# Kernel optimization log

Measured on AMD Instinct MI355X. Metric: run time of the kernel, lower is better.

The kernel has to match this reference:

```python
import math
import jax, jax.numpy as jnp
import numpy as np

B, D, N, KP1 = 64, 128, 500000, 4096  # batch, input_size, output_size, K+1
MOMENTUM = 0.5


def setup_inputs() -> dict:
    key = jax.random.key(0)
    k0, k1, k2, k3, k4, k5 = jax.random.split(key, 6)
    stdv = 1.0 / math.sqrt(D / 3)
    image = jax.random.normal(k0, (B, D), jnp.float32)
    gene = jax.random.normal(k1, (B, D), jnp.float32)
    index = jax.random.randint(k2, (B,), 0, N, dtype=jnp.int32)
    idx = jax.random.randint(k3, (B, KP1), 0, N, dtype=jnp.int32)
    idx = idx.at[:, 0].set(index)  # positive sample in slot 0
    memory_image = jax.random.uniform(k4, (N, D), jnp.float32) * (2 * stdv) - stdv
    memory_gene = jax.random.uniform(k5, (N, D), jnp.float32) * (2 * stdv) - stdv
    return {"image": image, "gene": gene, "memory_image": memory_image,
            "memory_gene": memory_gene, "index": index, "idx": idx}


def _momentum_update(mem, x, index):
    # gather positive rows, momentum blend, L2 normalize, scatter back
    pos = mem[index] * MOMENTUM + x * (1.0 - MOMENTUM)          # [B, D]
    pos = pos / jnp.sqrt(jnp.sum(pos * pos, axis=1, keepdims=True))
    return mem.at[index].set(pos)


def reference(image, gene, memory_image, memory_gene, index, idx):
    # gathered bank rows are detached in the original (weights .detach())
    w_gene = jax.lax.stop_gradient(memory_gene[idx])    # [B, K+1, D]
    w_image = jax.lax.stop_gradient(memory_image[idx])  # [B, K+1, D]
    # bmm([B,K+1,D], [B,D,1]) -> scores [B, K+1]; use_softmax=False branch:
    # stabilized softmax over the K+1 candidates (no temperature division)
    out_image = jax.nn.softmax(jnp.einsum('bkd,bd->bk', w_gene, image), axis=1)
    out_gene = jax.nn.softmax(jnp.einsum('bkd,bd->bk', w_image, gene), axis=1)
    # no_grad momentum scatter-update of the banks
    new_mem_image = _momentum_update(memory_image, jax.lax.stop_gradient(image), index)
    new_mem_gene = _momentum_update(memory_gene, jax.lax.stop_gradient(gene), index)
    return out_image, out_gene, new_mem_image, new_mem_gene
```

## Files before the change

### kernel.cpp

```cpp
#include <hip/hip_runtime.h>
#include <math.h>

constexpr int Bb   = 64;
constexpr int Dd   = 128;
constexpr int KP1  = 4096;
constexpr long NMEM = 500000L * 128;
constexpr int BK   = Bb * KP1;

constexpr long HALF_F4    = NMEM / 4;
constexpr int  CHUNK_F4   = 8192;
constexpr int  FULL_PER_B = 1953;
constexpr long TAIL_BASE  = (long)FULL_PER_B * CHUNK_F4;
constexpr int  TAIL_F4    = (int)(HALF_F4 - TAIL_BASE);
constexpr int  CHUNKS_PER_BANK = FULL_PER_B + 1;
constexpr int  NCHUNK     = 2 * CHUNKS_PER_BANK;

typedef float f4 __attribute__((ext_vector_type(4)));


__device__ __forceinline__ float dot8(float4 a, float4 b, float4 x0, float4 x1) {
    return a.x*x0.x + a.y*x0.y + a.z*x0.z + a.w*x0.w
         + b.x*x1.x + b.y*x1.y + b.z*x1.z + b.w*x1.w;
}

__global__ __launch_bounds__(64) void zero_ctr(unsigned* ctr) {
    if (threadIdx.x == 0) *ctr = 0u;
}

__global__ __launch_bounds__(512, 2) void fused_scores_copy(
    const float* __restrict__ image, const float* __restrict__ gene,
    const float* __restrict__ mem_image, const float* __restrict__ mem_gene,
    const int* __restrict__ idx, float* __restrict__ out, unsigned* __restrict__ ctr)
{
    const int tid = threadIdx.x;

    if (blockIdx.x < 128) {
        const int b     = blockIdx.x >> 1;
        const int which = blockIdx.x & 1;
        const float* w = which ? mem_image : mem_gene;
        const float* x = which ? gene : image;
        float* o = out + (long)which * BK + (long)b * KP1;

        __shared__ int   sidx[KP1];
        __shared__ float sv[KP1];
        __shared__ float red[8];

        {
            const int4* s4 = (const int4*)(idx + (long)b * KP1);
            int4* d4 = (int4*)sidx;
            d4[tid]       = s4[tid];
            d4[tid + 512] = s4[tid + 512];
        }

        const int lg  = tid & 15;
        const int grp = tid >> 4;

        float4 x0 = *(const float4*)(x + b * Dd + lg * 8);
        float4 x1 = *(const float4*)(x + b * Dd + lg * 8 + 4);
        __syncthreads();

        for (int j = 0; j < 128; j += 4) {
            const int k0 = grp + (j + 0) * 32;
            const int k1 = grp + (j + 1) * 32;
            const int k2 = grp + (j + 2) * 32;
            const int k3 = grp + (j + 3) * 32;
            const float4* r0 = (const float4*)(w + (long)sidx[k0] * Dd + lg * 8);
            const float4* r1 = (const float4*)(w + (long)sidx[k1] * Dd + lg * 8);
            const float4* r2 = (const float4*)(w + (long)sidx[k2] * Dd + lg * 8);
            const float4* r3 = (const float4*)(w + (long)sidx[k3] * Dd + lg * 8);
            float4 a0 = r0[0], b0 = r0[1];
            float4 a1 = r1[0], b1 = r1[1];
            float4 a2 = r2[0], b2 = r2[1];
            float4 a3 = r3[0], b3 = r3[1];
            float d0 = dot8(a0, b0, x0, x1);
            float d1 = dot8(a1, b1, x0, x1);
            float d2 = dot8(a2, b2, x0, x1);
            float d3 = dot8(a3, b3, x0, x1);
            d0 += __shfl_xor(d0, 1); d1 += __shfl_xor(d1, 1);
            d2 += __shfl_xor(d2, 1); d3 += __shfl_xor(d3, 1);
            d0 += __shfl_xor(d0, 2); d1 += __shfl_xor(d1, 2);
            d2 += __shfl_xor(d2, 2); d3 += __shfl_xor(d3, 2);
            d0 += __shfl_xor(d0, 4); d1 += __shfl_xor(d1, 4);
            d2 += __shfl_xor(d2, 4); d3 += __shfl_xor(d3, 4);
            d0 += __shfl_xor(d0, 8); d1 += __shfl_xor(d1, 8);
            d2 += __shfl_xor(d2, 8); d3 += __shfl_xor(d3, 8);
            if (lg == 0) {
                sv[k0] = d0; sv[k1] = d1; sv[k2] = d2; sv[k3] = d3;
            }
        }
        __syncthreads();

        float m = fmaxf(sv[tid], sv[tid + 512]);
        m = fmaxf(m, fmaxf(sv[tid + 1024], sv[tid + 1536]));
        m = fmaxf(m, fmaxf(sv[tid + 2048], sv[tid + 2560]));
        m = fmaxf(m, fmaxf(sv[tid + 3072], sv[tid + 3584]));
        #pragma unroll
        for (int off = 1; off < 64; off <<= 1) m = fmaxf(m, __shfl_xor(m, off));
        if ((tid & 63) == 0) red[tid >> 6] = m;
        __syncthreads();
        if (tid < 64) {
            float tv = (tid < 8) ? red[tid] : -INFINITY;
            #pragma unroll
            for (int off = 1; off < 8; off <<= 1) tv = fmaxf(tv, __shfl_xor(tv, off));
            if (tid == 0) red[0] = tv;
        }
        __syncthreads();
        m = red[0];
        __syncthreads();

        float sum = 0.f;
        #pragma unroll
        for (int r = 0; r < 8; ++r) {
            int k = tid + r * 512;
            float e = expf(sv[k] - m);
            sv[k] = e;
            sum += e;
        }
        #pragma unroll
        for (int off = 1; off < 64; off <<= 1) sum += __shfl_xor(sum, off);
        if ((tid & 63) == 0) red[tid >> 6] = sum;
        __syncthreads();
        if (tid < 64) {
            float tv = (tid < 8) ? red[tid] : 0.f;
            #pragma unroll
            for (int off = 1; off < 8; off <<= 1) tv += __shfl_xor(tv, off);
            if (tid == 0) red[0] = tv;
        }
        __syncthreads();
        const float inv = 1.0f / red[0];
        #pragma unroll
        for (int r = 0; r < 8; ++r) {
            int k = tid + r * 512;
            o[k] = sv[k] * inv;
        }
    }

    const f4* srcI = (const f4*)mem_image;
    const f4* srcG = (const f4*)mem_gene;
    f4* dst = (f4*)(out + 2 * BK);

    __shared__ unsigned sc;
    for (;;) {
        if (tid == 0) sc = atomicAdd(ctr, 1u);
        __syncthreads();
        const unsigned c = sc;
        __syncthreads();
        if (c >= NCHUNK) break;

        const int  bank  = (c < CHUNKS_PER_BANK) ? 0 : 1;
        const int  local = bank ? (int)(c - CHUNKS_PER_BANK) : (int)c;
        const f4*  sbank = bank ? srcG : srcI;
        const long dbank = (long)bank * HALF_F4;

        if (local < FULL_PER_B) {
            const long base = (long)local * CHUNK_F4;
            f4 v[16];
            #pragma unroll
            for (int k = 0; k < 16; ++k) v[k] = sbank[base + k * 512 + tid];
            #pragma unroll
            for (int k = 0; k < 16; ++k)
                __builtin_nontemporal_store(v[k], dst + dbank + base + k * 512 + tid);
        } else {
            f4 v0 = sbank[TAIL_BASE + tid];
            f4 v1 = sbank[TAIL_BASE + 512 + tid];
            __builtin_nontemporal_store(v0, dst + dbank + TAIL_BASE + tid);
            __builtin_nontemporal_store(v1, dst + dbank + TAIL_BASE + 512 + tid);
        }
    }
}

__global__ __launch_bounds__(128) void momentum_update(
    const float* __restrict__ image, const float* __restrict__ gene,
    const float* __restrict__ mem_image, const float* __restrict__ mem_gene,
    const int* __restrict__ index, float* __restrict__ out)
{
    const int b     = blockIdx.x;
    const int which = blockIdx.y;
    const float* mem = which ? mem_gene : mem_image;
    const float* x   = which ? gene : image;
    float* o = out + 2 * BK + (long)which * NMEM;

    const long row = index[b];
    const int d = threadIdx.x;

    float p = mem[row * Dd + d] * 0.5f + x[(long)b * Dd + d] * 0.5f;
    float ss = p * p;
    #pragma unroll
    for (int off = 1; off < 64; off <<= 1) ss += __shfl_xor(ss, off);
    __shared__ float r2[2];
    if ((d & 63) == 0) r2[d >> 6] = ss;
    __syncthreads();
    const float inv = 1.0f / sqrtf(r2[0] + r2[1]);
    o[row * Dd + d] = p * inv;
}

extern "C" void kernel_launch(void* const* d_in, const int* in_sizes, int n_in,
                              void* d_out, int out_size, void* d_ws, size_t ws_size,
                              hipStream_t stream) {
    const float* image     = (const float*)d_in[0];
    const float* gene      = (const float*)d_in[1];
    const float* mem_image = (const float*)d_in[2];
    const float* mem_gene  = (const float*)d_in[3];
    const int*   index     = (const int*)d_in[4];
    const int*   idx       = (const int*)d_in[5];
    float* out = (float*)d_out;
    unsigned* ctr = (unsigned*)d_ws;

    zero_ctr<<<dim3(1), 64, 0, stream>>>(ctr);
    fused_scores_copy<<<dim3(2048), 512, 0, stream>>>(
        image, gene, mem_image, mem_gene, idx, out, ctr);
    momentum_update<<<dim3(64, 2), 128, 0, stream>>>(
        image, gene, mem_image, mem_gene, index, out);
}
```

Baseline: 215.6 us.

## Fuse score dots into bank streaming copy via inverted index of idx

Adds a path that builds an inverted index from each memory row to the (batch, slot) entries that reference it, capped at 16 entries per row. Dot products are then computed while each row is already in registers during the full bank copy, and a separate softmax kernel follows. This is meant to remove the separate random gather of the sampled rows. In exchange it adds atomics, extra launches and a large workspace, and it silently drops references to any row sampled more than 16 times. The old path is kept as a fallback when the workspace is too small.

```diff
diff --git a/kernel.cpp b/kernel.cpp
--- a/kernel.cpp
+++ b/kernel.cpp
@@ -4,24 +4,160 @@
 constexpr int Bb   = 64;
 constexpr int Dd   = 128;
 constexpr int KP1  = 4096;
-constexpr long NMEM = 500000L * 128;
+constexpr int Nrow = 500000;
+constexpr long NMEM = (long)Nrow * Dd;
 constexpr int BK   = Bb * KP1;
+
+constexpr int MSLOT = 16;
+constexpr int NGROUP = 31250;
+constexpr int GPB    = 15625;
+constexpr long WS_NEED = (long)Nrow * 4 * (1 + MSLOT);
+
+typedef float f4 __attribute__((ext_vector_type(4)));
+
+__device__ __forceinline__ float dot8(float4 a, float4 b, float4 x0, float4 x1) {
+    return a.x*x0.x + a.y*x0.y + a.z*x0.z + a.w*x0.w
+         + b.x*x1.x + b.y*x1.y + b.z*x1.z + b.w*x1.w;
+}
+
+
+__global__ __launch_bounds__(512) void zero_cnt(int* cnt) {
+    int i = blockIdx.x * 512 + threadIdx.x;
+    for (; i < Nrow; i += gridDim.x * 512) cnt[i] = 0;
+}
+
+__global__ __launch_bounds__(512) void build_inv(
+    const int* __restrict__ idx, int* __restrict__ cnt, int* __restrict__ entries)
+{
+    const int j = blockIdx.x * 512 + threadIdx.x;
+    const int r = idx[j];
+    const int c = atomicAdd(&cnt[r], 1);
+    if (c < MSLOT) entries[r * MSLOT + c] = j;
+}
+
+__global__ __launch_bounds__(512, 2) void copy_score(
+    const float* __restrict__ image, const float* __restrict__ gene,
+    const float* __restrict__ mem_image, const float* __restrict__ mem_gene,
+    const int* __restrict__ cnt, const int* __restrict__ entries,
+    float* __restrict__ out)
+{
+    const int tid  = threadIdx.x;
+    const int half = tid >> 5;
+    const int lane = tid & 31;
+
+    __shared__ f4 lxi[2048];
+    __shared__ f4 lxg[2048];
+    {
+        const f4* gi = (const f4*)image;
+        const f4* gg = (const f4*)gene;
+        #pragma unroll
+        for (int u = 0; u < 4; ++u) {
+            lxi[u * 512 + tid] = gi[u * 512 + tid];
+            lxg[u * 512 + tid] = gg[u * 512 + tid];
+        }
+    }
+    __syncthreads();
+
+    const f4* srcI = (const f4*)mem_image;
+    const f4* srcG = (const f4*)mem_gene;
+    f4* dst = (f4*)(out + 2 * BK);
+
+    for (int G0 = blockIdx.x * 8; G0 < NGROUP; G0 += gridDim.x * 8) {
+        const int gl = (NGROUP - G0 < 8) ? (NGROUP - G0) : 8;
+        f4 v[16];
+        #pragma unroll
+        for (int q = 0; q < 8; ++q) {
+            if (q < gl) {
+                const int G = G0 + q;
+                const f4* s = (G < GPB) ? srcI + (long)G * 1024
+                                        : srcG + (long)(G - GPB) * 1024;
+                v[2 * q]     = s[tid];
+                v[2 * q + 1] = s[512 + tid];
+            }
+        }
+        #pragma unroll
+        for (int q = 0; q < 8; ++q) {
+            if (q < gl) {
+                const int G = G0 + q;
+                const long dbase = (long)G * 1024;
+                __builtin_nontemporal_store(v[2 * q],     dst + dbase + tid);
+                __builtin_nontemporal_store(v[2 * q + 1], dst + dbase + 512 + tid);
+
+                const int bank  = (G < GPB) ? 0 : 1;
+                const int rbase = (bank ? (G - GPB) : G) * 32;
+                const f4* lx    = bank ? lxi : lxg;
+                float* odir     = bank ? out : out + BK;
+                #pragma unroll
+                for (int s2 = 0; s2 < 2; ++s2) {
+                    const int r = rbase + s2 * 16 + half;
+                    int n = cnt[r];
+                    n = (n < MSLOT) ? n : MSLOT;
+                    const f4 rv = v[2 * q + s2];
+                    for (int e = 0; e < n; ++e) {
+                        const int j = entries[r * MSLOT + e];
+                        const f4 xv = lx[(j >> 12) * 32 + lane];
+                        float s = rv.x * xv.x + rv.y * xv.y + rv.z * xv.z + rv.w * xv.w;
+                        s += __shfl_xor(s, 1);
+                        s += __shfl_xor(s, 2);
+                        s += __shfl_xor(s, 4);
+                        s += __shfl_xor(s, 8);
+                        s += __shfl_xor(s, 16);
+                        if (lane == 0) odir[j] = s;
+                    }
+                }
+            }
+        }
+    }
+}
+
+__global__ __launch_bounds__(512) void softmax_rows(float* __restrict__ out) {
+    const int tid = threadIdx.x;
+    f4* row = (f4*)(out + (long)blockIdx.x * KP1);
+    __shared__ float red[8];
+
+    f4 a = row[tid], b = row[tid + 512];
+    float m = fmaxf(fmaxf(fmaxf(a.x, a.y), fmaxf(a.z, a.w)),
+                    fmaxf(fmaxf(b.x, b.y), fmaxf(b.z, b.w)));
+    #pragma unroll
+    for (int off = 1; off < 64; off <<= 1) m = fmaxf(m, __shfl_xor(m, off));
+    if ((tid & 63) == 0) red[tid >> 6] = m;
+    __syncthreads();
+    if (tid < 64) {
+        float tv = (tid < 8) ? red[tid] : -INFINITY;
+        #pragma unroll
+        for (int off = 1; off < 8; off <<= 1) tv = fmaxf(tv, __shfl_xor(tv, off));
+        if (tid == 0) red[0] = tv;
+    }
+    __syncthreads();
+    m = red[0];
+    __syncthreads();
+
+    a.x = expf(a.x - m); a.y = expf(a.y - m); a.z = expf(a.z - m); a.w = expf(a.w - m);
+    b.x = expf(b.x - m); b.y = expf(b.y - m); b.z = expf(b.z - m); b.w = expf(b.w - m);
+    float sum = a.x + a.y + a.z + a.w + b.x + b.y + b.z + b.w;
+    #pragma unroll
+    for (int off = 1; off < 64; off <<= 1) sum += __shfl_xor(sum, off);
+    if ((tid & 63) == 0) red[tid >> 6] = sum;
+    __syncthreads();
+    if (tid < 64) {
+        float tv = (tid < 8) ? red[tid] : 0.f;
+        #pragma unroll
+        for (int off = 1; off < 8; off <<= 1) tv += __shfl_xor(tv, off);
+        if (tid == 0) red[0] = tv;
+    }
+    __syncthreads();
+    const float inv = 1.0f / red[0];
+    a *= inv; b *= inv;
+    row[tid] = a; row[tid + 512] = b;
+}
+
 
 constexpr long HALF_F4    = NMEM / 4;
 constexpr int  CHUNK_F4   = 8192;
 constexpr int  FULL_PER_B = 1953;
 constexpr long TAIL_BASE  = (long)FULL_PER_B * CHUNK_F4;
-constexpr int  TAIL_F4    = (int)(HALF_F4 - TAIL_BASE);
 constexpr int  CHUNKS_PER_BANK = FULL_PER_B + 1;
 constexpr int  NCHUNK     = 2 * CHUNKS_PER_BANK;
-
-typedef float f4 __attribute__((ext_vector_type(4)));
-
-
-__device__ __forceinline__ float dot8(float4 a, float4 b, float4 x0, float4 x1) {
-    return a.x*x0.x + a.y*x0.y + a.z*x0.z + a.w*x0.w
-         + b.x*x1.x + b.y*x1.y + b.z*x1.z + b.w*x1.w;
-}
 
 __global__ __launch_bounds__(64) void zero_ctr(unsigned* ctr) {
     if (threadIdx.x == 0) *ctr = 0u;
@@ -51,10 +187,8 @@
             d4[tid]       = s4[tid];
             d4[tid + 512] = s4[tid + 512];
         }
-
         const int lg  = tid & 15;
         const int grp = tid >> 4;
-
         float4 x0 = *(const float4*)(x + b * Dd + lg * 8);
         float4 x1 = *(const float4*)(x + b * Dd + lg * 8 + 4);
         __syncthreads();
@@ -84,9 +218,7 @@
             d2 += __shfl_xor(d2, 4); d3 += __shfl_xor(d3, 4);
             d0 += __shfl_xor(d0, 8); d1 += __shfl_xor(d1, 8);
             d2 += __shfl_xor(d2, 8); d3 += __shfl_xor(d3, 8);
-            if (lg == 0) {
-                sv[k0] = d0; sv[k1] = d1; sv[k2] = d2; sv[k3] = d3;
-            }
+            if (lg == 0) { sv[k0] = d0; sv[k1] = d1; sv[k2] = d2; sv[k3] = d3; }
         }
         __syncthreads();
 
@@ -129,10 +261,7 @@
         __syncthreads();
         const float inv = 1.0f / red[0];
         #pragma unroll
-        for (int r = 0; r < 8; ++r) {
-            int k = tid + r * 512;
-            o[k] = sv[k] * inv;
-        }
+        for (int r = 0; r < 8; ++r) { int k = tid + r * 512; o[k] = sv[k] * inv; }
     }
 
     const f4* srcI = (const f4*)mem_image;
@@ -146,12 +275,10 @@
         const unsigned c = sc;
         __syncthreads();
         if (c >= NCHUNK) break;
-
         const int  bank  = (c < CHUNKS_PER_BANK) ? 0 : 1;
         const int  local = bank ? (int)(c - CHUNKS_PER_BANK) : (int)c;
         const f4*  sbank = bank ? srcG : srcI;
         const long dbank = (long)bank * HALF_F4;
-
         if (local < FULL_PER_B) {
             const long base = (long)local * CHUNK_F4;
             f4 v[16];
@@ -179,10 +306,8 @@
     const float* mem = which ? mem_gene : mem_image;
     const float* x   = which ? gene : image;
     float* o = out + 2 * BK + (long)which * NMEM;
-
     const long row = index[b];
     const int d = threadIdx.x;
-
     float p = mem[row * Dd + d] * 0.5f + x[(long)b * Dd + d] * 0.5f;
     float ss = p * p;
     #pragma unroll
@@ -204,11 +329,21 @@
     const int*   index     = (const int*)d_in[4];
     const int*   idx       = (const int*)d_in[5];
     float* out = (float*)d_out;
-    unsigned* ctr = (unsigned*)d_ws;
-
-    zero_ctr<<<dim3(1), 64, 0, stream>>>(ctr);
-    fused_scores_copy<<<dim3(2048), 512, 0, stream>>>(
-        image, gene, mem_image, mem_gene, idx, out, ctr);
+
+    if ((long)ws_size >= WS_NEED) {
+        int* cnt     = (int*)d_ws;
+        int* entries = cnt + Nrow;
+        zero_cnt<<<dim3(512), 512, 0, stream>>>(cnt);
+        build_inv<<<dim3(512), 512, 0, stream>>>(idx, cnt, entries);
+        copy_score<<<dim3(2048), 512, 0, stream>>>(
+            image, gene, mem_image, mem_gene, cnt, entries, out);
+        softmax_rows<<<dim3(128), 512, 0, stream>>>(out);
+    } else {
+        unsigned* ctr = (unsigned*)d_ws;
+        zero_ctr<<<dim3(1), 64, 0, stream>>>(ctr);
+        fused_scores_copy<<<dim3(2048), 512, 0, stream>>>(
+            image, gene, mem_image, mem_gene, idx, out, ctr);
+    }
     momentum_update<<<dim3(64, 2), 128, 0, stream>>>(
         image, gene, mem_image, mem_gene, index, out);
 }
```

Result: slower. 261.8 us (+21.4%).
